# Kernel tuning notes

Measured on AMD Instinct MI355X. Metric: run time of the kernel, lower is better.

## Reference

```python
import jax, jax.numpy as jnp
import numpy as np

EPS = 1e-5
RATES = (1, 6, 12, 18)


def _bn(x, g, b, m, v):
    # eval-mode BatchNorm2d: x [B,C,H,W], params [C]
    inv = g / jnp.sqrt(v + EPS)
    return x * inv[None, :, None, None] + (b - m * inv)[None, :, None, None]


def setup_inputs() -> dict:
    key = jax.random.key(0)
    ks = jax.random.split(key, 20)
    B, C, H, W = 8, 512, 96, 96
    Cq = C // 4  # 128 channels per branch, depthwise (groups=128)
    f32 = jnp.float32
    inp = {}
    inp["x"] = jax.random.normal(ks[0], (B, C, H, W), f32)
    # four depthwise 3x3 conv branches (stacked over branch axis)
    inp["wdw"] = jax.random.normal(ks[1], (4, Cq, 1, 3, 3), f32) * 0.1
    inp["bdw"] = jax.random.normal(ks[2], (4, Cq), f32) * 0.01
    inp["gdw"] = jnp.ones((4, Cq), f32) + 0.1 * jax.random.normal(ks[3], (4, Cq), f32)
    inp["bedw"] = jax.random.normal(ks[4], (4, Cq), f32) * 0.01
    inp["mdw"] = jax.random.normal(ks[5], (4, Cq), f32) * 0.01
    inp["vdw"] = jax.random.uniform(ks[6], (4, Cq), f32, 0.5, 1.5)
    # out_s: shared 1x1 conv 4->4 + bn(4)
    inp["ws"] = jax.random.normal(ks[7], (4, 4, 1, 1), f32) * 0.5
    inp["bs"] = jax.random.normal(ks[8], (4,), f32) * 0.01
    inp["gs"] = jnp.ones((4,), f32) + 0.1 * jax.random.normal(ks[9], (4,), f32)
    inp["bes"] = jax.random.normal(ks[10], (4,), f32) * 0.01
    inp["ms"] = jax.random.normal(ks[11], (4,), f32) * 0.01
    inp["vs"] = jax.random.uniform(ks[12], (4,), f32, 0.5, 1.5)
    # out: 1x1 conv 512->512 + bn(512)
    inp["wo"] = jax.random.normal(ks[13], (C, C, 1, 1), f32) * (1.0 / np.sqrt(C))
    inp["bo"] = jax.random.normal(ks[14], (C,), f32) * 0.01
    inp["go"] = jnp.ones((C,), f32) + 0.1 * jax.random.normal(ks[15], (C,), f32)
    inp["beo"] = jax.random.normal(ks[16], (C,), f32) * 0.01
    inp["mo"] = jax.random.normal(ks[17], (C,), f32) * 0.01
    inp["vo"] = jax.random.uniform(ks[18], (C,), f32, 0.5, 1.5)
    return inp


def reference(x, wdw, bdw, gdw, bedw, mdw, vdw, ws, bs, gs, bes, ms, vs,
              wo, bo, go, beo, mo, vo):
    B = x.shape[0]
    Cq = wdw.shape[1]  # 128
    xs = jnp.split(x, 4, axis=1)  # four [B,Cq,H,W] chunks
    branches = []
    for i, r in enumerate(RATES):
        y = jax.lax.conv_general_dilated(
            xs[i], wdw[i], window_strides=(1, 1),
            padding=[(r, r), (r, r)], rhs_dilation=(r, r),
            dimension_numbers=("NCHW", "OIHW", "NCHW"),
            feature_group_count=Cq)
        y = y + bdw[i][None, :, None, None]
        y = jax.nn.relu(_bn(y, gdw[i], bedw[i], mdw[i], vdw[i]))
        branches.append(y)
    # Per-channel loop in the original == shared 1x1 conv over the branch axis.
    z = jnp.stack(branches, axis=2)  # [B, Cq, 4, H, W]
    W4 = ws[:, :, 0, 0]  # [4,4]
    z = jnp.einsum("oi,bcihw->bcohw", W4, z) + bs[None, None, :, None, None]
    inv_s = gs / jnp.sqrt(vs + EPS)
    z = jax.nn.relu(z * inv_s[None, None, :, None, None]
                    + (bes - ms * inv_s)[None, None, :, None, None])
    # concat order: channel c contributes its 4 out_s channels consecutively
    z = z.reshape(B, Cq * 4, z.shape[3], z.shape[4])  # [B,512,H,W]
    # final 1x1 conv 512->512 + bn + relu
    Wo = wo[:, :, 0, 0]
    out = jnp.einsum("oi,bihw->bohw", Wo, z) + bo[None, :, None, None]
    out = jax.nn.relu(_bn(out, go, beo, mo, vo))
    return out
```

## Files before the change

### kernel.cpp

```cpp
#include <hip/hip_runtime.h>
#include <cstdint>
#include <cstddef>

typedef float  f32x4 __attribute__((ext_vector_type(4)));
typedef float  f32x2 __attribute__((ext_vector_type(2)));
typedef short  s16x8 __attribute__((ext_vector_type(8)));
typedef short  s16x4 __attribute__((ext_vector_type(4)));
typedef unsigned int u32x4 __attribute__((ext_vector_type(4)));

#define EPSV 1e-5f

__device__ __forceinline__ float rfl(float v) {
  return __builtin_bit_cast(float, __builtin_amdgcn_readfirstlane(__builtin_bit_cast(int, v)));
}
__device__ __forceinline__ unsigned pk2(float a, float b) {
  unsigned short ua = __builtin_bit_cast(unsigned short, (__bf16)a);
  unsigned short ub = __builtin_bit_cast(unsigned short, (__bf16)b);
  return (unsigned)ua | ((unsigned)ub << 16);
}
__device__ __forceinline__ void gll16(const void* g, void* l) {
  __builtin_amdgcn_global_load_lds((const __attribute__((address_space(1))) unsigned int*)g,
                                   (__attribute__((address_space(3))) unsigned int*)l, 16, 0, 0);
}
__device__ __forceinline__ f32x4 relu4(f32x4 v) {
  f32x4 r; r.x = fmaxf(v.x,0.f); r.y = fmaxf(v.y,0.f); r.z = fmaxf(v.z,0.f); r.w = fmaxf(v.w,0.f);
  return r;
}

__global__ void kF(const float* __restrict__ wo, const float* __restrict__ bo,
                   const float* __restrict__ go, const float* __restrict__ beo,
                   const float* __restrict__ mo, const float* __restrict__ vo,
                   __bf16* __restrict__ wopp, float* __restrict__ co)
{
  const int oc = blockIdx.x;
  const int k  = threadIdx.x;
  float invo = go[oc] * rsqrtf(vo[oc] + EPSV);
  float v = wo[(size_t)oc*512 + k] * invo;
  int mt = oc >> 7, ocl = oc & 127;
  int kt = k >> 6, kk = (k >> 5) & 1, g = (k >> 3) & 3, jj = k & 7;
  size_t dst = (size_t)(mt*8 + kt)*10240 + (size_t)kk*5120 + ocl*40 + g*8 + jj;
  wopp[dst] = (__bf16)v;
  if (k == 0) co[oc] = bo[oc]*invo + beo[oc] - mo[oc]*invo;
}

__global__ __launch_bounds__(1024) void kA(const float* __restrict__ x,
    const float* __restrict__ wdw, const float* __restrict__ bdw, const float* __restrict__ gdw,
    const float* __restrict__ bedw, const float* __restrict__ mdw, const float* __restrict__ vdw,
    const float* __restrict__ w4, const float* __restrict__ bsc, const float* __restrict__ gsc,
    const float* __restrict__ besc, const float* __restrict__ msc, const float* __restrict__ vsc,
    __bf16* __restrict__ z2s)
{
  __shared__ alignas(16) float lds[32 + 4*9216 + 32];
  const int tid = threadIdx.x;
  const int b = blockIdx.x >> 7, c = blockIdx.x & 127;

  {
    const f32x4* xv = (const f32x4*)x;
    f32x4* lv = (f32x4*)(lds + 32);
    const size_t base = (size_t)(b*512 + c) * 2304;
    #pragma unroll
    for (int kq = 0; kq < 9; ++kq) {
      int j = tid + kq*1024;
      int i = j / 2304;
      int off = j - i*2304;
      lv[j] = xv[base + (size_t)i*128*2304 + off];
    }
  }

  float wf[4][9], cdwv[4], w4f[4][4], c4v[4];
  #pragma unroll
  for (int i = 0; i < 4; ++i) {
    int idx = i*128 + c;
    float inv = gdw[idx] * rsqrtf(vdw[idx] + EPSV);
    #pragma unroll
    for (int t = 0; t < 9; ++t) wf[i][t] = rfl(wdw[(size_t)idx*9 + t] * inv);
    cdwv[i] = rfl(bdw[idx]*inv + bedw[idx] - mdw[idx]*inv);
  }
  #pragma unroll
  for (int o = 0; o < 4; ++o) {
    float invs = gsc[o] * rsqrtf(vsc[o] + EPSV);
    #pragma unroll
    for (int i = 0; i < 4; ++i) w4f[o][i] = rfl(w4[o*4 + i] * invs);
    c4v[o] = rfl(bsc[o]*invs + besc[o] - msc[o]*invs);
  }

  __syncthreads();

  const int RR[4] = {1, 6, 12, 18};
  __bf16* zbase = z2s + (size_t)(b*128 + c) * 36864;

  for (int q = tid; q < 2304; q += 1024) {
    int h = q / 24;
    int w0 = (q - h*24) * 4;
    f32x4 y[4];
    #pragma unroll
    for (int i = 0; i < 4; ++i) {
      const int r = RR[i];
      f32x4 mL, mR;
      #pragma unroll
      for (int j = 0; j < 4; ++j) {
        mL[j] = (w0 + j - r >= 0) ? 1.f : 0.f;
        mR[j] = (w0 + j + r <= 95) ? 1.f : 0.f;
      }
      f32x4 acc = {0.f, 0.f, 0.f, 0.f};
      #pragma unroll
      for (int dh = -1; dh <= 1; ++dh) {
        int h2 = h + dh*r;
        if ((unsigned)h2 < 96u) {
          const float* row = lds + 32 + i*9216 + h2*96 + w0;
          f32x4 tc = *(const f32x4*)row;
          f32x4 tl, tr;
          if (r == 1) {
            float sm = row[-1], sp = row[4];
            tl = (f32x4){sm, tc.x, tc.y, tc.z};
            tr = (f32x4){tc.y, tc.z, tc.w, sp};
          } else if (r == 12) {
            tl = *(const f32x4*)(row - 12);
            tr = *(const f32x4*)(row + 12);
          } else {
            f32x2 a0 = *(const f32x2*)(row - r);
            f32x2 a1 = *(const f32x2*)(row - r + 2);
            f32x2 b0 = *(const f32x2*)(row + r);
            f32x2 b1 = *(const f32x2*)(row + r + 2);
            tl = (f32x4){a0.x, a0.y, a1.x, a1.y};
            tr = (f32x4){b0.x, b0.y, b1.x, b1.y};
          }
          const int wb = (dh + 1) * 3;
          acc += wf[i][wb+0]*(tl*mL) + wf[i][wb+1]*tc + wf[i][wb+2]*(tr*mR);
        }
      }
      y[i] = relu4(acc + cdwv[i]);
    }
    f32x4 z[4];
    #pragma unroll
    for (int o = 0; o < 4; ++o) {
      f32x4 t = {c4v[o], c4v[o], c4v[o], c4v[o]};
      #pragma unroll
      for (int i = 0; i < 4; ++i) t += w4f[o][i]*y[i];
      z[o] = relu4(t);
    }
    u32x4 s0 = { pk2(z[0].x,z[1].x), pk2(z[2].x,z[3].x), pk2(z[0].y,z[1].y), pk2(z[2].y,z[3].y) };
    u32x4 s1 = { pk2(z[0].z,z[1].z), pk2(z[2].z,z[3].z), pk2(z[0].w,z[1].w), pk2(z[2].w,z[3].w) };
    u32x4* dst = (u32x4*)(zbase + (size_t)q*16);
    dst[0] = s0;
    dst[1] = s1;
  }
}

__global__ __launch_bounds__(256) void kB(const void* __restrict__ wopp_,
    const void* __restrict__ z2s_, const float* __restrict__ co, float* __restrict__ out)
{
  __shared__ alignas(16) char lA[20480];
  __shared__ alignas(16) char lB[16384];
  const char* wopp = (const char*)wopp_;
  const char* z2s  = (const char*)z2s_;

  const int tid = threadIdx.x;
  const int lane = tid & 63, wv = tid >> 6;
  const int wm = wv >> 1, wn = wv & 1;
  const int pt = blockIdx.x;
  const int mt = blockIdx.y;
  const int b  = blockIdx.z;
  const int pix0 = pt * 128;
  const int l15 = lane & 15, lg = lane >> 4;

  f32x4 acc[4][4] = {};

  for (int kt = 0; kt < 8; ++kt) {
    const char* srcA = wopp + (size_t)(mt*8 + kt)*20480;
    for (int j = wv; j < 20; j += 4)
      gll16(srcA + j*1024 + lane*16, lA + j*1024);
    #pragma unroll
    for (int ct4 = 0; ct4 < 4; ++ct4) {
      int ct = wv*4 + ct4;
      const char* srcB = z2s + ((size_t)(b*128 + kt*16 + ct)*36864 + (size_t)pix0*4)*2;
      gll16(srcB + lane*16, lB + ct*1024);
    }
    __syncthreads();

    #pragma unroll
    for (int kk = 0; kk < 2; ++kk) {
      s16x8 af[4];
      #pragma unroll
      for (int m = 0; m < 4; ++m)
        af[m] = *(const s16x8*)(lA + kk*10240 + (wm*64 + m*16 + l15)*80 + lg*16);
      #pragma unroll
      for (int n = 0; n < 4; ++n) {
        const char* p = lB + kk*8192 + lg*2048 + (wn*64 + n*16 + l15)*8;
        s16x4 lo = *(const s16x4*)(p);
        s16x4 hi = *(const s16x4*)(p + 1024);
        s16x8 bfr = __builtin_shufflevector(lo, hi, 0,1,2,3,4,5,6,7);
        #pragma unroll
        for (int m = 0; m < 4; ++m)
          acc[m][n] = __builtin_amdgcn_mfma_f32_16x16x32_bf16(af[m], bfr, acc[m][n], 0, 0, 0);
      }
    }
    __syncthreads();
  }

  const int colp = pix0 + wn*64 + l15;
  #pragma unroll
  for (int m = 0; m < 4; ++m) {
    const int ocb = mt*128 + wm*64 + m*16 + lg*4;
    #pragma unroll
    for (int r2 = 0; r2 < 4; ++r2) {
      const int oc = ocb + r2;
      const float cov = co[oc];
      float* orow = out + ((size_t)(b*512 + oc))*9216 + colp;
      #pragma unroll
      for (int n = 0; n < 4; ++n) {
        float v = acc[m][n][r2] + cov;
        orow[(size_t)n*16] = fmaxf(v, 0.f);
      }
    }
  }
}

extern "C" void kernel_launch(void* const* d_in, const int* in_sizes, int n_in,
                              void* d_out, int out_size, void* d_ws, size_t ws_size,
                              hipStream_t stream)
{
  (void)in_sizes; (void)out_size;
  if (n_in < 19) return;
  const size_t Z2_BYTES = 75497472;
  const size_t WOPP_BYTES = 655360;
  if (ws_size < Z2_BYTES + WOPP_BYTES + 2048) return;

  const float* x    = (const float*)d_in[0];
  const float* wdw  = (const float*)d_in[1];
  const float* bdw  = (const float*)d_in[2];
  const float* gdw  = (const float*)d_in[3];
  const float* bedw = (const float*)d_in[4];
  const float* mdw  = (const float*)d_in[5];
  const float* vdw  = (const float*)d_in[6];
  const float* w4   = (const float*)d_in[7];
  const float* bs   = (const float*)d_in[8];
  const float* gs   = (const float*)d_in[9];
  const float* bes  = (const float*)d_in[10];
  const float* ms   = (const float*)d_in[11];
  const float* vs   = (const float*)d_in[12];
  const float* wo   = (const float*)d_in[13];
  const float* bo   = (const float*)d_in[14];
  const float* go   = (const float*)d_in[15];
  const float* beo  = (const float*)d_in[16];
  const float* mo   = (const float*)d_in[17];
  const float* vo   = (const float*)d_in[18];

  __bf16* z2s  = (__bf16*)d_ws;
  __bf16* wopp = (__bf16*)((char*)d_ws + Z2_BYTES);
  float*  co   = (float*)((char*)d_ws + Z2_BYTES + WOPP_BYTES);

  kF<<<512, 512, 0, stream>>>(wo, bo, go, beo, mo, vo, wopp, co);
  kA<<<1024, 1024, 0, stream>>>(x, wdw, bdw, gdw, bedw, mdw, vdw, w4, bs, gs, bes, ms, vs, z2s);
  kB<<<dim3(72, 4, 8), 256, 0, stream>>>(wopp, z2s, co, (float*)d_out);
}
```

Baseline: 145.6 us.

## Stream depthwise branches through a single zero-padded LDS plane in kA

Instead of staging all four 96x96 branch planes in LDS (about 147KB per block), kA now loads one branch plane at a time into a zero-padded 96x136 buffer (about 52KB) and accumulates the 4x4 mixing into registers across branches. The zero padding removes the per-tap edge masks, and the block shrinks to 768 threads with each thread owning 3 rows of a 4-wide column strip. The smaller LDS footprint is meant to let several blocks share a CU and raise occupancy. In exchange there are extra __syncthreads per branch, the global loads are serialized per branch without prefetch, and each thread holds more accumulator registers.

```diff
diff --git a/kernel.cpp b/kernel.cpp
--- a/kernel.cpp
+++ b/kernel.cpp
@@ -43,29 +43,16 @@
   if (k == 0) co[oc] = bo[oc]*invo + beo[oc] - mo[oc]*invo;
 }
 
-__global__ __launch_bounds__(1024) void kA(const float* __restrict__ x,
+__global__ __launch_bounds__(768, 6) void kA(const float* __restrict__ x,
     const float* __restrict__ wdw, const float* __restrict__ bdw, const float* __restrict__ gdw,
     const float* __restrict__ bedw, const float* __restrict__ mdw, const float* __restrict__ vdw,
     const float* __restrict__ w4, const float* __restrict__ bsc, const float* __restrict__ gsc,
     const float* __restrict__ besc, const float* __restrict__ msc, const float* __restrict__ vsc,
     __bf16* __restrict__ z2s)
 {
-  __shared__ alignas(16) float lds[32 + 4*9216 + 32];
+  __shared__ alignas(16) float sp[96*136];
   const int tid = threadIdx.x;
   const int b = blockIdx.x >> 7, c = blockIdx.x & 127;
-
-  {
-    const f32x4* xv = (const f32x4*)x;
-    f32x4* lv = (f32x4*)(lds + 32);
-    const size_t base = (size_t)(b*512 + c) * 2304;
-    #pragma unroll
-    for (int kq = 0; kq < 9; ++kq) {
-      int j = tid + kq*1024;
-      int i = j / 2304;
-      int off = j - i*2304;
-      lv[j] = xv[base + (size_t)i*128*2304 + off];
-    }
-  }
 
   float wf[4][9], cdwv[4], w4f[4][4], c4v[4];
   #pragma unroll
@@ -84,64 +71,87 @@
     c4v[o] = rfl(bsc[o]*invs + besc[o] - msc[o]*invs);
   }
 
-  __syncthreads();
+  for (int z = tid; z < 96*40; z += 768) {
+    int row = z / 40, cw = z - row*40;
+    sp[row*136 + (cw < 20 ? cw : 96 + cw)] = 0.f;
+  }
+
+  const int wq = tid % 24;
+  const int hb = (tid / 24) * 3;
+  const int w0 = wq * 4;
+
+  const f32x4* xv = (const f32x4*)x;
+  const size_t gbase = (size_t)(b*512 + c) * 2304;
+
+  int srow[3], scol[3];
+  #pragma unroll
+  for (int k = 0; k < 3; ++k) { int g = tid + k*768; srow[k] = g/24; scol[k] = g - srow[k]*24; }
+
+  f32x4 zacc[4][3];
+  #pragma unroll
+  for (int o = 0; o < 4; ++o)
+    #pragma unroll
+    for (int k = 0; k < 3; ++k)
+      zacc[o][k] = (f32x4){c4v[o], c4v[o], c4v[o], c4v[o]};
 
   const int RR[4] = {1, 6, 12, 18};
-  __bf16* zbase = z2s + (size_t)(b*128 + c) * 36864;
-
-  for (int q = tid; q < 2304; q += 1024) {
-    int h = q / 24;
-    int w0 = (q - h*24) * 4;
-    f32x4 y[4];
-    #pragma unroll
-    for (int i = 0; i < 4; ++i) {
-      const int r = RR[i];
-      f32x4 mL, mR;
-      #pragma unroll
-      for (int j = 0; j < 4; ++j) {
-        mL[j] = (w0 + j - r >= 0) ? 1.f : 0.f;
-        mR[j] = (w0 + j + r <= 95) ? 1.f : 0.f;
-      }
+
+  #pragma unroll
+  for (int i = 0; i < 4; ++i) {
+    __syncthreads();
+    #pragma unroll
+    for (int k = 0; k < 3; ++k) {
+      f32x4 v = xv[gbase + (size_t)i*294912 + (size_t)(tid + k*768)];
+      *(f32x4*)(sp + srow[k]*136 + 20 + scol[k]*4) = v;
+    }
+    __syncthreads();
+
+    const int r = RR[i];
+    #pragma unroll
+    for (int k = 0; k < 3; ++k) {
+      const int h = hb + k;
       f32x4 acc = {0.f, 0.f, 0.f, 0.f};
       #pragma unroll
       for (int dh = -1; dh <= 1; ++dh) {
-        int h2 = h + dh*r;
+        const int h2 = h + dh*r;
         if ((unsigned)h2 < 96u) {
-          const float* row = lds + 32 + i*9216 + h2*96 + w0;
+          const float* row = sp + h2*136 + 20 + w0;
           f32x4 tc = *(const f32x4*)row;
           f32x4 tl, tr;
-          if (r == 1) {
-            float sm = row[-1], sp = row[4];
-            tl = (f32x4){sm, tc.x, tc.y, tc.z};
-            tr = (f32x4){tc.y, tc.z, tc.w, sp};
+          if (i == 0) {
+            f32x2 a  = *(const f32x2*)(row - 2);
+            f32x2 bb = *(const f32x2*)(row + 4);
+            tl = (f32x4){a.y, tc.x, tc.y, tc.z};
+            tr = (f32x4){tc.y, tc.z, tc.w, bb.x};
           } else if (r == 12) {
             tl = *(const f32x4*)(row - 12);
             tr = *(const f32x4*)(row + 12);
           } else {
-            f32x2 a0 = *(const f32x2*)(row - r);
-            f32x2 a1 = *(const f32x2*)(row - r + 2);
-            f32x2 b0 = *(const f32x2*)(row + r);
-            f32x2 b1 = *(const f32x2*)(row + r + 2);
+            f32x2 a0 = *(const f32x2*)(row - r), a1 = *(const f32x2*)(row - r + 2);
+            f32x2 b0 = *(const f32x2*)(row + r), b1 = *(const f32x2*)(row + r + 2);
             tl = (f32x4){a0.x, a0.y, a1.x, a1.y};
             tr = (f32x4){b0.x, b0.y, b1.x, b1.y};
           }
           const int wb = (dh + 1) * 3;
-          acc += wf[i][wb+0]*(tl*mL) + wf[i][wb+1]*tc + wf[i][wb+2]*(tr*mR);
+          acc += wf[i][wb]*tl + wf[i][wb+1]*tc + wf[i][wb+2]*tr;
         }
       }
-      y[i] = relu4(acc + cdwv[i]);
-    }
+      f32x4 y = relu4(acc + cdwv[i]);
+      #pragma unroll
+      for (int o = 0; o < 4; ++o) zacc[o][k] += w4f[o][i]*y;
+    }
+  }
+
+  __bf16* zbase = z2s + (size_t)(b*128 + c) * 36864;
+  #pragma unroll
+  for (int k = 0; k < 3; ++k) {
+    const int h = hb + k;
     f32x4 z[4];
     #pragma unroll
-    for (int o = 0; o < 4; ++o) {
-      f32x4 t = {c4v[o], c4v[o], c4v[o], c4v[o]};
-      #pragma unroll
-      for (int i = 0; i < 4; ++i) t += w4f[o][i]*y[i];
-      z[o] = relu4(t);
-    }
+    for (int o = 0; o < 4; ++o) z[o] = relu4(zacc[o][k]);
     u32x4 s0 = { pk2(z[0].x,z[1].x), pk2(z[2].x,z[3].x), pk2(z[0].y,z[1].y), pk2(z[2].y,z[3].y) };
     u32x4 s1 = { pk2(z[0].z,z[1].z), pk2(z[2].z,z[3].z), pk2(z[0].w,z[1].w), pk2(z[2].w,z[3].w) };
-    u32x4* dst = (u32x4*)(zbase + (size_t)q*16);
+    u32x4* dst = (u32x4*)(zbase + (size_t)(h*24 + wq)*16);
     dst[0] = s0;
     dst[1] = s1;
   }
@@ -251,6 +261,6 @@
   float*  co   = (float*)((char*)d_ws + Z2_BYTES + WOPP_BYTES);
 
   kF<<<512, 512, 0, stream>>>(wo, bo, go, beo, mo, vo, wopp, co);
-  kA<<<1024, 1024, 0, stream>>>(x, wdw, bdw, gdw, bedw, mdw, vdw, w4, bs, gs, bes, ms, vs, z2s);
+  kA<<<1024, 768, 0, stream>>>(x, wdw, bdw, gdw, bedw, mdw, vdw, w4, bs, gs, bes, ms, vs, z2s);
   kB<<<dim3(72, 4, 8), 256, 0, stream>>>(wopp, z2s, co, (float*)d_out);
 }
```

After: 124.8 us. -14.3%, faster.
